# Kernel optimization log

Measured on AMD Instinct MI355X. Metric: run time of the kernel, lower is better.

Reference implementation:

```python
import jax, jax.numpy as jnp
import numpy as np

B, S, D = 64, 4096, 512


def setup_inputs() -> dict:
    key = jax.random.key(0)
    k1, k2, k3 = jax.random.split(key, 3)
    topic_embedding = jax.random.normal(k1, (B, D), dtype=jnp.float32)
    sequence_embedding = jax.random.normal(k2, (B, S, D), dtype=jnp.float32)
    # tfr Bilinear(D, D, output_dim=1): score = emb1^T W emb2 + bias
    W = jax.random.normal(k3, (D, D), dtype=jnp.float32) / np.sqrt(D)
    bias = jnp.zeros((1,), dtype=jnp.float32)
    return {"topic_embedding": topic_embedding,
            "sequence_embedding": sequence_embedding,
            "W": W, "bias": bias}


def reference(topic_embedding, sequence_embedding, W, bias):
    # Original: repeat topic over seq dim, map_fn over batch applying
    # bilinear(topic, token) then softmax over tokens. Vectorized:
    # factor the bilinear form: score[b,s] = (topic[b] @ W) . seq[b,s] + bias
    t = topic_embedding @ W                                  # [B, D]
    scores = jnp.einsum('bd,bsd->bs', t, sequence_embedding) + bias  # [B, S]
    beta = jax.nn.softmax(scores, axis=-1)                   # [B, S]
    return beta
```

## Files before the change

### kernel.cpp

```cpp
#include <hip/hip_runtime.h>
#include <math.h>

#define BB 64
#define SS 4096
#define DD 512

__global__ __launch_bounds__(256) void tW_kernel(const float* __restrict__ topic,
                                                 const float* __restrict__ W,
                                                 float* __restrict__ t) {
    __shared__ float tp[DD];
    __shared__ float4 part[256];
    const int b      = blockIdx.x >> 2;
    const int dchunk = (blockIdx.x & 3) * 32;
    const int dg     = threadIdx.x & 31;
    const int strip  = threadIdx.x >> 5;
    for (int i = threadIdx.x; i < DD; i += 256) tp[i] = topic[b * DD + i];
    __syncthreads();
    const float4* W4 = (const float4*)W;
    float4 acc = {0.f, 0.f, 0.f, 0.f};
    const int k0 = strip * 64;
#pragma unroll 8
    for (int k = 0; k < 64; ++k) {
        const float s  = tp[k0 + k];
        const float4 w = W4[(size_t)(k0 + k) * 128 + dchunk + dg];
        acc.x += s * w.x; acc.y += s * w.y; acc.z += s * w.z; acc.w += s * w.w;
    }
    part[threadIdx.x] = acc;
    __syncthreads();
    if (threadIdx.x < 32) {
        float4 r = part[threadIdx.x];
#pragma unroll
        for (int st = 1; st < 8; ++st) {
            const float4 q = part[st * 32 + threadIdx.x];
            r.x += q.x; r.y += q.y; r.z += q.z; r.w += q.w;
        }
        ((float4*)(t + b * DD))[dchunk + dg] = r;
    }
}

__global__ __launch_bounds__(256) void scores_kernel(const float* __restrict__ t,
                                                     const float* __restrict__ seq,
                                                     const float* __restrict__ bias,
                                                     float* __restrict__ scores) {
    const int b    = blockIdx.y;
    const int s0   = blockIdx.x << 5;
    const int wave = threadIdx.x >> 6;
    const int lane = threadIdx.x & 63;

    const float4* trow = (const float4*)(t + b * DD);
    const float4 ta = trow[lane];
    const float4 tb = trow[lane + 64];
    const float bs = bias[0];

    const float4* base = (const float4*)(seq + ((size_t)b * SS + s0) * DD);
    float* srow = scores + (size_t)b * SS + s0;

#pragma unroll
    for (int j = 0; j < 8; j += 2) {
        const int i0 = wave + 4 * j;
        const int i1 = i0 + 4;
        const float4* p0 = base + (size_t)i0 * 128;
        const float4* p1 = base + (size_t)i1 * 128;
        const float4 a0 = p0[lane], c0 = p0[lane + 64];
        const float4 a1 = p1[lane], c1 = p1[lane + 64];
        float r0 = a0.x * ta.x + a0.y * ta.y + a0.z * ta.z + a0.w * ta.w
                 + c0.x * tb.x + c0.y * tb.y + c0.z * tb.z + c0.w * tb.w;
        float r1 = a1.x * ta.x + a1.y * ta.y + a1.z * ta.z + a1.w * ta.w
                 + c1.x * tb.x + c1.y * tb.y + c1.z * tb.z + c1.w * tb.w;
#pragma unroll
        for (int m = 32; m; m >>= 1) {
            r0 += __shfl_xor(r0, m, 64);
            r1 += __shfl_xor(r1, m, 64);
        }
        if (lane == 0) {
            srow[i0] = r0 + bs;
            srow[i1] = r1 + bs;
        }
    }
}

__global__ __launch_bounds__(1024) void softmax_kernel(const float* __restrict__ scores,
                                                       float* __restrict__ out) {
    __shared__ float red[16];
    const int b   = blockIdx.x;
    const int tid = threadIdx.x;
    const int wave = tid >> 6, lane = tid & 63;

    const float4 v = ((const float4*)(scores + (size_t)b * SS))[tid];

    float m = fmaxf(fmaxf(v.x, v.y), fmaxf(v.z, v.w));
#pragma unroll
    for (int k = 32; k; k >>= 1) m = fmaxf(m, __shfl_xor(m, k, 64));
    if (lane == 0) red[wave] = m;
    __syncthreads();
    if (tid < 16) {
        float x = red[tid];
#pragma unroll
        for (int k = 8; k; k >>= 1) x = fmaxf(x, __shfl_xor(x, k, 16));
        if (tid == 0) red[0] = x;
    }
    __syncthreads();
    m = red[0];
    __syncthreads();

    float4 e;
    e.x = __expf(v.x - m); e.y = __expf(v.y - m);
    e.z = __expf(v.z - m); e.w = __expf(v.w - m);
    float s = e.x + e.y + e.z + e.w;
#pragma unroll
    for (int k = 32; k; k >>= 1) s += __shfl_xor(s, k, 64);
    if (lane == 0) red[wave] = s;
    __syncthreads();
    if (tid < 16) {
        float x = red[tid];
#pragma unroll
        for (int k = 8; k; k >>= 1) x += __shfl_xor(x, k, 16);
        if (tid == 0) red[0] = x;
    }
    __syncthreads();
    const float inv = 1.f / red[0];

    float4 o;
    o.x = e.x * inv; o.y = e.y * inv; o.z = e.z * inv; o.w = e.w * inv;
    ((float4*)(out + (size_t)b * SS))[tid] = o;
}

extern "C" void kernel_launch(void* const* d_in, const int* in_sizes, int n_in,
                              void* d_out, int out_size, void* d_ws, size_t ws_size,
                              hipStream_t stream) {
    const float* topic = (const float*)d_in[0];
    const float* seq   = (const float*)d_in[1];
    const float* W     = (const float*)d_in[2];
    const float* bias  = (const float*)d_in[3];
    float* out = (float*)d_out;

    float* t      = (float*)d_ws;
    float* scores = t + BB * DD;

    tW_kernel<<<dim3(BB * 4), 256, 0, stream>>>(topic, W, t);
    scores_kernel<<<dim3(SS / 32, BB), 256, 0, stream>>>(t, seq, bias, scores);
    softmax_kernel<<<dim3(BB), 1024, 0, stream>>>(scores, out);
}
```

Baseline: 683.6 us.

## Remap scores kernel to 4 lanes per row with shared-memory topic vector

The scores kernel now gives each sequence row to a group of 4 lanes instead of a full wavefront. Each lane walks 128 of the row's floats with float4 loads, so only a 2-step shuffle reduction is needed. The topic vector t is staged in shared memory, and each block now covers 64 rows instead of 32, which halves the grid. The intent is to cut the cross-wave shuffle overhead. The risk is that global loads become strided: each group of 4 lanes reads 64 contiguous bytes per load, with consecutive groups 2KB apart, which may hurt coalescing on a kernel that is bandwidth-bound.

```diff
diff --git a/kernel.cpp b/kernel.cpp
--- a/kernel.cpp
+++ b/kernel.cpp
@@ -42,41 +42,38 @@
                                                      const float* __restrict__ seq,
                                                      const float* __restrict__ bias,
                                                      float* __restrict__ scores) {
-    const int b    = blockIdx.y;
-    const int s0   = blockIdx.x << 5;
-    const int wave = threadIdx.x >> 6;
-    const int lane = threadIdx.x & 63;
+    __shared__ float4 tsh[128];
+    const int b = blockIdx.y;
+    if (threadIdx.x < 128) tsh[threadIdx.x] = ((const float4*)(t + b * DD))[threadIdx.x];
+    __syncthreads();
 
-    const float4* trow = (const float4*)(t + b * DD);
-    const float4 ta = trow[lane];
-    const float4 tb = trow[lane + 64];
-    const float bs = bias[0];
+    const int wave    = threadIdx.x >> 6;
+    const int lane    = threadIdx.x & 63;
+    const int d_part  = lane & 3;
+    const int s_local = lane >> 2;
+    const int s       = (blockIdx.x * 4 + wave) * 16 + s_local;
 
-    const float4* base = (const float4*)(seq + ((size_t)b * SS + s0) * DD);
-    float* srow = scores + (size_t)b * SS + s0;
+    const float4* row = (const float4*)(seq + ((size_t)b * SS + s) * DD);
 
-#pragma unroll
-    for (int j = 0; j < 8; j += 2) {
-        const int i0 = wave + 4 * j;
-        const int i1 = i0 + 4;
-        const float4* p0 = base + (size_t)i0 * 128;
-        const float4* p1 = base + (size_t)i1 * 128;
-        const float4 a0 = p0[lane], c0 = p0[lane + 64];
-        const float4 a1 = p1[lane], c1 = p1[lane + 64];
-        float r0 = a0.x * ta.x + a0.y * ta.y + a0.z * ta.z + a0.w * ta.w
-                 + c0.x * tb.x + c0.y * tb.y + c0.z * tb.z + c0.w * tb.w;
-        float r1 = a1.x * ta.x + a1.y * ta.y + a1.z * ta.z + a1.w * ta.w
-                 + c1.x * tb.x + c1.y * tb.y + c1.z * tb.z + c1.w * tb.w;
-#pragma unroll
-        for (int m = 32; m; m >>= 1) {
-            r0 += __shfl_xor(r0, m, 64);
-            r1 += __shfl_xor(r1, m, 64);
-        }
-        if (lane == 0) {
-            srow[i0] = r0 + bs;
-            srow[i1] = r1 + bs;
-        }
+    float a0 = 0.f, a1 = 0.f, a2 = 0.f, a3 = 0.f;
+    for (int j = 0; j < 32; j += 4) {
+        const float4 v0 = row[(j + 0) * 4 + d_part];
+        const float4 v1 = row[(j + 1) * 4 + d_part];
+        const float4 v2 = row[(j + 2) * 4 + d_part];
+        const float4 v3 = row[(j + 3) * 4 + d_part];
+        const float4 t0 = tsh[(j + 0) * 4 + d_part];
+        const float4 t1 = tsh[(j + 1) * 4 + d_part];
+        const float4 t2 = tsh[(j + 2) * 4 + d_part];
+        const float4 t3 = tsh[(j + 3) * 4 + d_part];
+        a0 += v0.x * t0.x + v0.y * t0.y + v0.z * t0.z + v0.w * t0.w;
+        a1 += v1.x * t1.x + v1.y * t1.y + v1.z * t1.z + v1.w * t1.w;
+        a2 += v2.x * t2.x + v2.y * t2.y + v2.z * t2.z + v2.w * t2.w;
+        a3 += v3.x * t3.x + v3.y * t3.y + v3.z * t3.z + v3.w * t3.w;
     }
+    float partial = (a0 + a1) + (a2 + a3);
+    partial += __shfl_xor(partial, 1, 64);
+    partial += __shfl_xor(partial, 2, 64);
+    if (d_part == 0) scores[(size_t)b * SS + s] = partial + bias[0];
 }
 
 __global__ __launch_bounds__(1024) void softmax_kernel(const float* __restrict__ scores,
@@ -138,6 +135,6 @@
     float* scores = t + BB * DD;
 
     tW_kernel<<<dim3(BB * 4), 256, 0, stream>>>(topic, W, t);
-    scores_kernel<<<dim3(SS / 32, BB), 256, 0, stream>>>(t, seq, bias, scores);
+    scores_kernel<<<dim3(SS / 64, BB), 256, 0, stream>>>(t, seq, bias, scores);
     softmax_kernel<<<dim3(BB), 1024, 0, stream>>>(scores, out);
 }
```

Result: no change. 683.9 us (+0.1%).
